# Performance work log

Hardware: AMD Instinct MI355X
Metric: run time of the kernel (lower is better)

The kernel has to match this reference:

```python
import jax, jax.numpy as jnp
import numpy as np

B, C, N, D = 8, 4, 1024, 96
H, DK, DV = 3, 32, 32
EPS = 1e-5


def setup_inputs() -> dict:
    key = jax.random.key(0)
    ks = jax.random.split(key, 7)
    s = 1.0 / np.sqrt(D)
    return {
        "input_Q": jax.random.normal(ks[0], (B, C, N, D), jnp.float32),
        "input_K": jax.random.normal(ks[1], (B, C, N, D), jnp.float32),
        "input_V": jax.random.normal(ks[2], (B, C, N, D), jnp.float32),
        "W_Q": jax.random.normal(ks[3], (H * DK, D), jnp.float32) * s,
        "W_K": jax.random.normal(ks[4], (H * DK, D), jnp.float32) * s,
        "W_V": jax.random.normal(ks[5], (H * DV, D), jnp.float32) * s,
        "W_fc": jax.random.normal(ks[6], (D, H * DV), jnp.float32) * s,
        "ln_gamma": jnp.ones((D,), jnp.float32),
        "ln_beta": jnp.zeros((D,), jnp.float32),
    }


def reference(input_Q, input_K, input_V, W_Q, W_K, W_V, W_fc, ln_gamma, ln_beta):
    # projections (torch Linear: x @ W.T), then split heads: [B,C,N,H*dk] -> [B,C,H,N,dk]
    def split_heads(x, W, dh):
        y = jnp.einsum('bcnd,ed->bcne', x, W)
        return y.reshape(B, C, N, H, dh).transpose(0, 1, 3, 2, 4)

    Q = split_heads(input_Q, W_Q, DK)
    K = split_heads(input_K, W_K, DK)
    V = split_heads(input_V, W_V, DV)

    scores = jnp.einsum('bchqd,bchkd->bchqk', Q, K) / np.sqrt(DK).astype(np.float32)
    # NOTE: original code softmaxes over dim=3 of the 5D scores == the QUERY axis
    attn = jax.nn.softmax(scores, axis=3)
    context = jnp.einsum('bchqk,bchkd->bchqd', attn, V)
    context = context.transpose(0, 1, 3, 2, 4).reshape(B, C, N, H * DV)

    out = jnp.einsum('bcne,de->bcnd', context, W_fc) + input_Q  # residual
    mu = jnp.mean(out, axis=-1, keepdims=True)
    var = jnp.var(out, axis=-1, keepdims=True)
    return (out - mu) * jax.lax.rsqrt(var + EPS) * ln_gamma + ln_beta
```

## Files before the change

kernel.cpp:

```cpp
#include <hip/hip_runtime.h>
#include <hip/hip_bf16.h>

#define NB 8
#define NC 4
#define NN 1024
#define ND 96
#define NHH 3
#define DKV 32
#define NBC (NB*NC)
#define NHEAD (NBC*NHH)
#define NROWS (NBC*NN)
#define C1 0.25503486910638953f
#define EPSV 1e-5f

using short8 = __attribute__((ext_vector_type(8))) short;
using sh4    = __attribute__((ext_vector_type(4))) short;
using f32x4  = __attribute__((ext_vector_type(4))) float;
using f32x16 = __attribute__((ext_vector_type(16))) float;

__device__ __forceinline__ short bf16_of(float f) {
  __hip_bfloat16 h = __float2bfloat16(f);
  return __builtin_bit_cast(short, h);
}
__device__ __forceinline__ float f_of_bf16(short s) {
  return __bfloat162float(__builtin_bit_cast(__hip_bfloat16, s));
}

__device__ __forceinline__ short8 load_cvt8(const float* p) {
  float4 f0 = *(const float4*)p;
  float4 f1 = *(const float4*)(p + 4);
  short8 v;
  v[0] = bf16_of(f0.x); v[1] = bf16_of(f0.y); v[2] = bf16_of(f0.z); v[3] = bf16_of(f0.w);
  v[4] = bf16_of(f1.x); v[5] = bf16_of(f1.y); v[6] = bf16_of(f1.z); v[7] = bf16_of(f1.w);
  return v;
}

__device__ __forceinline__ void gload_lds16(const void* g, void* l) {
  __builtin_amdgcn_global_load_lds(
      (const __attribute__((address_space(1))) unsigned int*)g,
      (__attribute__((address_space(3))) unsigned int*)l,
      16, 0, 0);
}

__global__ __launch_bounds__(256) void proj_kernel(
    const float* __restrict__ xq, const float* __restrict__ xk, const float* __restrict__ xv,
    const float* __restrict__ Wq, const float* __restrict__ Wk, const float* __restrict__ Wv,
    short* __restrict__ qb, short* __restrict__ kb, short* __restrict__ vb)
{
  __shared__ __align__(16) short wlds[96][104];
  __shared__ __align__(16) short xlds[64][104];
  const int t = threadIdx.x;
  const int p = blockIdx.x >> 9;
  const int blkrow0 = (blockIdx.x & 511) * 64;

  const float* x = (p == 0) ? xq : (p == 1) ? xk : xv;
  const float* W = (p == 0) ? Wq : (p == 1) ? Wk : Wv;
  short* dst = (p == 0) ? qb : (p == 1) ? kb : vb;
  const float sc = (p == 1) ? C1 : 1.0f;

#pragma unroll
  for (int i = 0; i < 9; ++i) {
    const int idx = i*256 + t;
    const float4 wv = *(const float4*)(W + (size_t)idx*4);
    const int f = idx*4, row = f/96, col = f%96;
    sh4 w4;
    w4[0] = bf16_of(wv.x); w4[1] = bf16_of(wv.y);
    w4[2] = bf16_of(wv.z); w4[3] = bf16_of(wv.w);
    *(sh4*)&wlds[row][col] = w4;
  }
#pragma unroll
  for (int it = 0; it < 3; ++it) {
    const int f = it*2048 + t*8;
    const int row = f / 96, col = f % 96;
    *(short8*)&xlds[row][col] = load_cvt8(x + (size_t)(blkrow0 + row)*ND + col);
  }
  __syncthreads();

  const int wave = t >> 6, lane = t & 63;
  const int g = lane >> 4, li = lane & 15;
  const int acol = g * 8;

  const short8 a0 = *(const short8*)&xlds[wave*16 + li][acol];
  const short8 a1 = *(const short8*)&xlds[wave*16 + li][32 + acol];
  const short8 a2 = *(const short8*)&xlds[wave*16 + li][64 + acol];

  f32x4 oacc[6];
#pragma unroll
  for (int tt = 0; tt < 6; ++tt) {
    f32x4 acc = {0.f, 0.f, 0.f, 0.f};
    const short* wr = &wlds[tt*16 + li][acol];
    acc = __builtin_amdgcn_mfma_f32_16x16x32_bf16(a0, *(const short8*)(wr),      acc, 0, 0, 0);
    acc = __builtin_amdgcn_mfma_f32_16x16x32_bf16(a1, *(const short8*)(wr + 32), acc, 0, 0, 0);
    acc = __builtin_amdgcn_mfma_f32_16x16x32_bf16(a2, *(const short8*)(wr + 64), acc, 0, 0, 0);
    oacc[tt] = acc;
  }

#pragma unroll
  for (int tt = 0; tt < 6; ++tt)
#pragma unroll
    for (int r = 0; r < 4; ++r)
      xlds[wave*16 + g*4 + r][tt*16 + li] = bf16_of(oacc[tt][r] * sc);
  __syncthreads();

#pragma unroll
  for (int it = 0; it < 3; ++it) {
    const int task = it*256 + t;
    const int nn_l = task / 12, seg = task - nn_l*12;
    const int col8 = seg*8;
    const int h = col8 >> 5, dd = col8 & 31;
    const int n = blkrow0 + nn_l;
    const int bcx = n >> 10, nnx = n & 1023;
    *(short8*)&dst[((size_t)(bcx*NHH + h)*NN + nnx)*DKV + dd] =
        *(const short8*)&xlds[nn_l][col8];
  }
}

__global__ __launch_bounds__(256) void stats_kernel(
    const short* __restrict__ qb, const short* __restrict__ kb,
    const short* __restrict__ vb, short* __restrict__ vtb)
{
  __shared__ __align__(16) short s_q[2][4096];
  __shared__ float s_is[128];
  __shared__ __align__(16) short s_t[32][128];

  const int t = threadIdx.x, wave = t >> 6, lane = t & 63;
  const int g = lane >> 4, li = lane & 15;
  const int head = blockIdx.x % NHEAD;
  const int kblk = blockIdx.x / NHEAD;
  const int kb0 = kblk*128;
  const int k0 = kb0 + wave*32;

  const short* kr = kb + ((size_t)head*NN + k0)*DKV + g*8;
  const short8 af0 = *(const short8*)(kr + (size_t)li*DKV);
  const short8 af1 = *(const short8*)(kr + (size_t)(16 + li)*DKV);

  const int nl = t >> 1;
  const int dvs = (t & 1) * 16;
  const short* vrow = vb + ((size_t)head*NN + kb0 + nl)*DKV + dvs;
  const short8 v0 = *(const short8*)(vrow);
  const short8 v1 = *(const short8*)(vrow + 8);

  const char* qsrc = (const char*)(qb + (size_t)head*NN*DKV);
  char* sq0 = (char*)&s_q[0][0];
  char* sq1 = (char*)&s_q[1][0];
  const int wseg = wave*2048;

  f32x4 s0 = {0.f,0.f,0.f,0.f}, s1 = {0.f,0.f,0.f,0.f};

#pragma unroll
  for (int j = 0; j < 2; ++j)
    gload_lds16(qsrc + wseg + j*1024 + lane*16, sq0 + wseg + j*1024);
  __syncthreads();

  for (int qc = 0; qc < 8; ++qc) {
    const int cur = qc & 1;
    const short* scur = (const short*)(cur ? sq1 : sq0);
    char* snxt = cur ? sq0 : sq1;
    if (qc < 7) {
#pragma unroll
      for (int j = 0; j < 2; ++j)
        gload_lds16(qsrc + (size_t)(qc+1)*8192 + wseg + j*1024 + lane*16,
                    snxt + wseg + j*1024);
    }
    __builtin_amdgcn_s_setprio(1);
#pragma unroll
    for (int qt = 0; qt < 8; ++qt) {
      const short8 bf = *(const short8*)(scur + (qt*16 + li)*32 + g*8);
      f32x4 z = {0.f,0.f,0.f,0.f};
      f32x4 d0 = __builtin_amdgcn_mfma_f32_16x16x32_bf16(af0, bf, z, 0, 0, 0);
      f32x4 d1 = __builtin_amdgcn_mfma_f32_16x16x32_bf16(af1, bf, z, 0, 0, 0);
#pragma unroll
      for (int r = 0; r < 4; ++r) {
        s0[r] += __builtin_amdgcn_exp2f(d0[r]);
        s1[r] += __builtin_amdgcn_exp2f(d1[r]);
      }
    }
    __builtin_amdgcn_s_setprio(0);
    __syncthreads();
  }

#pragma unroll
  for (int ms = 1; ms <= 8; ms <<= 1) {
#pragma unroll
    for (int r = 0; r < 4; ++r) {
      s0[r] += __shfl_xor(s0[r], ms);
      s1[r] += __shfl_xor(s1[r], ms);
    }
  }
  if (li == 0) {
    float* dst = s_is + wave*32 + g*4;
#pragma unroll
    for (int r = 0; r < 4; ++r) {
      dst[r]      = 1.0f / s0[r];
      dst[16 + r] = 1.0f / s1[r];
    }
  }
  __syncthreads();

  {
    const float isv = s_is[nl];
    short* st = &s_t[0][0];
#pragma unroll
    for (int j = 0; j < 8; ++j) {
      const int dv0 = dvs + j, dv1 = dvs + 8 + j;
      st[dv0*128 + (((nl*2) ^ ((dv0 & 7) << 4)) >> 1)] = bf16_of(isv * f_of_bf16(v0[j]));
      st[dv1*128 + (((nl*2) ^ ((dv1 & 7) << 4)) >> 1)] = bf16_of(isv * f_of_bf16(v1[j]));
    }
  }
  __syncthreads();

  {
    const short* st = &s_t[0][0];
#pragma unroll
    for (int it = 0; it < 2; ++it) {
      const int task = it*256 + t;
      const int dv = task >> 4, ns = task & 15;
      short8 v = *(const short8*)(st + dv*128 + (((ns*16) ^ ((dv & 7) << 4)) >> 1));
      *(short8*)(vtb + ((size_t)head*DKV + dv)*NN + kb0 + ns*8) = v;
    }
  }
}

__global__ __launch_bounds__(384) void ctxout_kernel(
    const short* __restrict__ qb, const short* __restrict__ kb,
    const short* __restrict__ vtb, const float* __restrict__ resid,
    const float* __restrict__ Wfc, const float* __restrict__ gamma,
    const float* __restrict__ beta, float* __restrict__ out)
{
  __shared__ __align__(16) char smem[49152];

  const int t = threadIdx.x;
  const int w = t >> 6, lane = t & 63;
  const int li = lane & 31, hi = lane >> 5;
  const int hs = t >> 7;
  const int sub = w & 1;
  const int bc = blockIdx.x % NBC;
  const int qtile = blockIdx.x / NBC;
  const int q0 = qtile*64 + sub*32;
  const int head = bc*NHH + hs;

  float4 wreg[6];
#pragma unroll
  for (int i = 0; i < 6; ++i)
    wreg[i] = *(const float4*)(Wfc + i*1536 + t*4);

  char* kbase = smem + hs*16384;
  char* vbase = kbase + 8192;

  const short* kgp = kb  + (size_t)head*NN*DKV;
  const short* vgp = vtb + (size_t)head*DKV*NN;
  const short* qrow = qb + ((size_t)head*NN + q0 + li)*DKV;
  const short8 qf0 = *(const short8*)(qrow + hi*8);
  const short8 qf1 = *(const short8*)(qrow + 16 + hi*8);

  int kgoff[2], vgoff[2], ldsseg[2];
#pragma unroll
  for (int j = 0; j < 2; ++j) {
    const int b = (sub*2 + j)*1024 + lane*16;
    const int r = b >> 7, c = b & 127;
    const int pc = c ^ ((r & 7) << 4);
    const int xk6 = r + 32*(pc >> 6);
    const int kr = (xk6 & 51) | ((xk6 & 4) << 1) | ((xk6 & 8) >> 1);
    kgoff[j] = kr*64 + (pc & 63);
    vgoff[j] = r*(NN*2) + pc;
    ldsseg[j] = (sub*2 + j)*1024;
  }

  int rd_off[2][2];
#pragma unroll
  for (int kt = 0; kt < 2; ++kt) {
    const int base = kt*64 + hi*16;
    rd_off[kt][0] = li*128 + ((base)      ^ ((li & 7) << 4));
    rd_off[kt][1] = li*128 + ((base + 32) ^ ((li & 7) << 4));
  }

  f32x16 acc = {0.f,0.f,0.f,0.f,0.f,0.f,0.f,0.f,0.f,0.f,0.f,0.f,0.f,0.f,0.f,0.f};

#pragma unroll
  for (int j = 0; j < 2; ++j) {
    gload_lds16((const char*)kgp + kgoff[j], kbase + ldsseg[j]);
    gload_lds16((const char*)vgp + vgoff[j], vbase + ldsseg[j]);
  }
  __syncthreads();

  for (int kc = 0; kc < 16; ++kc) {
    const int cur = kc & 1;
    if (kc < 15) {
      const size_t kadv = (size_t)(kc+1)*4096;
      const int vadv = (kc+1)*128;
#pragma unroll
      for (int j = 0; j < 2; ++j) {
        gload_lds16((const char*)kgp + kadv + kgoff[j],
                    kbase + (cur^1)*4096 + ldsseg[j]);
        gload_lds16((const char*)vgp + vadv + vgoff[j],
                    vbase + (cur^1)*4096 + ldsseg[j]);
      }
    }
    const char* kc_b = kbase + cur*4096;
    const char* vc_b = vbase + cur*4096;

    __builtin_amdgcn_s_setprio(1);
#pragma unroll
    for (int kt = 0; kt < 2; ++kt) {
      const short8 a0 = *(const short8*)(kc_b + rd_off[kt][0]);
      const short8 a1 = *(const short8*)(kc_b + rd_off[kt][1]);
      f32x16 sT = {0.f,0.f,0.f,0.f,0.f,0.f,0.f,0.f,0.f,0.f,0.f,0.f,0.f,0.f,0.f,0.f};
      sT = __builtin_amdgcn_mfma_f32_32x32x16_bf16(a0, qf0, sT, 0, 0, 0);
      sT = __builtin_amdgcn_mfma_f32_32x32x16_bf16(a1, qf1, sT, 0, 0, 0);
      short8 pa0, pa1;
#pragma unroll
      for (int j = 0; j < 8; ++j) {
        pa0[j] = bf16_of(__builtin_amdgcn_exp2f(sT[j]));
        pa1[j] = bf16_of(__builtin_amdgcn_exp2f(sT[8 + j]));
      }
      const short8 vfa = *(const short8*)(vc_b + rd_off[kt][0]);
      const short8 vfb = *(const short8*)(vc_b + rd_off[kt][1]);
      acc = __builtin_amdgcn_mfma_f32_32x32x16_bf16(pa0, vfa, acc, 0, 0, 0);
      acc = __builtin_amdgcn_mfma_f32_32x32x16_bf16(pa1, vfb, acc, 0, 0, 0);
    }
    __builtin_amdgcn_s_setprio(0);

    __syncthreads();
  }

  short* s_ct = (short*)smem;
  short* wlds = (short*)(smem + 13312);

#pragma unroll
  for (int reg = 0; reg < 16; ++reg) {
    const int ql = sub*32 + (reg & 3) + 8*(reg >> 2) + 4*hi;
    s_ct[ql*104 + hs*32 + li] = bf16_of(acc[reg]);
  }
#pragma unroll
  for (int i = 0; i < 6; ++i) {
    const int f = i*1536 + t*4;
    const int row = f / 96, col = f % 96;
    sh4 w4;
    w4[0] = bf16_of(wreg[i].x); w4[1] = bf16_of(wreg[i].y);
    w4[2] = bf16_of(wreg[i].z); w4[3] = bf16_of(wreg[i].w);
    *(sh4*)&wlds[row*104 + col] = w4;
  }
  __syncthreads();

  if (w < 4) {
    const int g16 = lane >> 4, li16 = lane & 15;
    const int rbase = w*16;
    const size_t rowg = (size_t)bc*NN + qtile*64 + rbase;

    const short* ar = s_ct + (rbase + li16)*104 + g16*8;
    const short8 a0 = *(const short8*)(ar);
    const short8 a1 = *(const short8*)(ar + 32);
    const short8 a2 = *(const short8*)(ar + 64);

    float o[6][4];
#pragma unroll
    for (int tt = 0; tt < 6; ++tt) {
      f32x4 oa = {0.f, 0.f, 0.f, 0.f};
      const short* wr = wlds + (tt*16 + li16)*104 + g16*8;
      oa = __builtin_amdgcn_mfma_f32_16x16x32_bf16(a0, *(const short8*)(wr),      oa, 0, 0, 0);
      oa = __builtin_amdgcn_mfma_f32_16x16x32_bf16(a1, *(const short8*)(wr + 32), oa, 0, 0, 0);
      oa = __builtin_amdgcn_mfma_f32_16x16x32_bf16(a2, *(const short8*)(wr + 64), oa, 0, 0, 0);
#pragma unroll
      for (int r = 0; r < 4; ++r)
        o[tt][r] = oa[r] + resid[(rowg + g16*4 + r)*ND + tt*16 + li16];
    }

    float s1v[4], s2v[4];
#pragma unroll
    for (int r = 0; r < 4; ++r) {
      float a = 0.f, b = 0.f;
#pragma unroll
      for (int tt = 0; tt < 6; ++tt) { a += o[tt][r]; b += o[tt][r]*o[tt][r]; }
      s1v[r] = a; s2v[r] = b;
    }
#pragma unroll
    for (int ms = 1; ms <= 8; ms <<= 1) {
#pragma unroll
      for (int r = 0; r < 4; ++r) {
        s1v[r] += __shfl_xor(s1v[r], ms);
        s2v[r] += __shfl_xor(s2v[r], ms);
      }
    }
    float mean[4], rs[4];
#pragma unroll
    for (int r = 0; r < 4; ++r) {
      mean[r] = s1v[r] * (1.0f/96.0f);
      float var = s2v[r]*(1.0f/96.0f) - mean[r]*mean[r];
      rs[r] = rsqrtf(var + EPSV);
    }
#pragma unroll
    for (int tt = 0; tt < 6; ++tt) {
      const int e = tt*16 + li16;
      const float gg = gamma[e], bb = beta[e];
#pragma unroll
      for (int r = 0; r < 4; ++r)
        out[(rowg + g16*4 + r)*ND + e] = (o[tt][r] - mean[r])*rs[r]*gg + bb;
    }
  }
}

extern "C" void kernel_launch(void* const* d_in, const int* in_sizes, int n_in,
                              void* d_out, int out_size, void* d_ws, size_t ws_size,
                              hipStream_t stream) {
  (void)in_sizes; (void)n_in; (void)out_size; (void)ws_size;
  const float* xq    = (const float*)d_in[0];
  const float* xk    = (const float*)d_in[1];
  const float* xv    = (const float*)d_in[2];
  const float* Wq    = (const float*)d_in[3];
  const float* Wk    = (const float*)d_in[4];
  const float* Wv    = (const float*)d_in[5];
  const float* Wfc   = (const float*)d_in[6];
  const float* gamma = (const float*)d_in[7];
  const float* beta  = (const float*)d_in[8];
  float* out = (float*)d_out;

  short* qb  = (short*)d_ws;
  short* kb  = qb  + (size_t)NHEAD*NN*DKV;
  short* vtb = kb  + (size_t)NHEAD*NN*DKV;
  short* vb  = vtb + (size_t)NHEAD*NN*DKV;

  hipLaunchKernelGGL(proj_kernel,   dim3(3*NROWS/64), dim3(256), 0, stream,
                     xq, xk, xv, Wq, Wk, Wv, qb, kb, vb);
  hipLaunchKernelGGL(stats_kernel,  dim3(NHEAD*8), dim3(256), 0, stream,
                     qb, kb, vb, vtb);
  hipLaunchKernelGGL(ctxout_kernel, dim3(NBC*16), dim3(384), 0, stream,
                     qb, kb, vtb, xq, Wfc, gamma, beta, out);
}
```

Measured before the change: 56.58 us.

## Triple-buffer K/V tiles in ctxout with prefetch distance two and vmcnt waits

Moves the attention-context kernel from double to triple buffering of K and V tiles in LDS, prefetching two chunks ahead. The full __syncthreads is replaced by a partial s_waitcnt vmcnt plus s_barrier, so one chunk's loads can stay in flight across the barrier. LDS per block grows from 48 KB to 72 KB through dynamic shared memory, which can lower the number of resident blocks per CU. Empty asm constraints pin the Wfc and Q registers so they are loaded early.

```diff
diff --git a/kernel.cpp b/kernel.cpp
--- a/kernel.cpp
+++ b/kernel.cpp
@@ -227,7 +227,7 @@
     const float* __restrict__ Wfc, const float* __restrict__ gamma,
     const float* __restrict__ beta, float* __restrict__ out)
 {
-  __shared__ __align__(16) char smem[49152];
+  extern __shared__ __align__(16) char smem[];
 
   const int t = threadIdx.x;
   const int w = t >> 6, lane = t & 63;
@@ -239,19 +239,23 @@
   const int q0 = qtile*64 + sub*32;
   const int head = bc*NHH + hs;
 
-  float4 wreg[6];
+  f32x4 wreg[6];
 #pragma unroll
   for (int i = 0; i < 6; ++i)
-    wreg[i] = *(const float4*)(Wfc + i*1536 + t*4);
-
-  char* kbase = smem + hs*16384;
-  char* vbase = kbase + 8192;
+    wreg[i] = *(const f32x4*)(Wfc + i*1536 + t*4);
+
+  char* kbase = smem + hs*24576;
+  char* vbase = kbase + 12288;
 
   const short* kgp = kb  + (size_t)head*NN*DKV;
   const short* vgp = vtb + (size_t)head*DKV*NN;
   const short* qrow = qb + ((size_t)head*NN + q0 + li)*DKV;
-  const short8 qf0 = *(const short8*)(qrow + hi*8);
-  const short8 qf1 = *(const short8*)(qrow + 16 + hi*8);
+  short8 qf0 = *(const short8*)(qrow + hi*8);
+  short8 qf1 = *(const short8*)(qrow + 16 + hi*8);
+
+#pragma unroll
+  for (int i = 0; i < 6; ++i) asm volatile("" : "+v"(wreg[i]));
+  asm volatile("" : "+v"(qf0), "+v"(qf1));
 
   int kgoff[2], vgoff[2], ldsseg[2];
 #pragma unroll
@@ -277,23 +281,30 @@
   f32x16 acc = {0.f,0.f,0.f,0.f,0.f,0.f,0.f,0.f,0.f,0.f,0.f,0.f,0.f,0.f,0.f,0.f};
 
 #pragma unroll
-  for (int j = 0; j < 2; ++j) {
-    gload_lds16((const char*)kgp + kgoff[j], kbase + ldsseg[j]);
-    gload_lds16((const char*)vgp + vgoff[j], vbase + ldsseg[j]);
-  }
-  __syncthreads();
+  for (int c = 0; c < 2; ++c) {
+    const size_t kadv = (size_t)c*4096;
+    const int vadv = c*128;
+#pragma unroll
+    for (int j = 0; j < 2; ++j) {
+      gload_lds16((const char*)kgp + kadv + kgoff[j], kbase + c*4096 + ldsseg[j]);
+      gload_lds16((const char*)vgp + vadv + vgoff[j], vbase + c*4096 + ldsseg[j]);
+    }
+  }
+  __builtin_amdgcn_sched_barrier(0);
+  asm volatile("s_waitcnt vmcnt(4)" ::: "memory");
+  __builtin_amdgcn_s_barrier();
+  __builtin_amdgcn_sched_barrier(0);
 
   for (int kc = 0; kc < 16; ++kc) {
-    const int cur = kc & 1;
-    if (kc < 15) {
-      const size_t kadv = (size_t)(kc+1)*4096;
-      const int vadv = (kc+1)*128;
+    const int cur = kc % 3;
+    if (kc < 14) {
+      const int nb = (kc + 2) % 3;
+      const size_t kadv = (size_t)(kc+2)*4096;
+      const int vadv = (kc+2)*128;
 #pragma unroll
       for (int j = 0; j < 2; ++j) {
-        gload_lds16((const char*)kgp + kadv + kgoff[j],
-                    kbase + (cur^1)*4096 + ldsseg[j]);
-        gload_lds16((const char*)vgp + vadv + vgoff[j],
-                    vbase + (cur^1)*4096 + ldsseg[j]);
+        gload_lds16((const char*)kgp + kadv + kgoff[j], kbase + nb*4096 + ldsseg[j]);
+        gload_lds16((const char*)vgp + vadv + vgoff[j], vbase + nb*4096 + ldsseg[j]);
       }
     }
     const char* kc_b = kbase + cur*4096;
@@ -320,7 +331,11 @@
     }
     __builtin_amdgcn_s_setprio(0);
 
-    __syncthreads();
+    __builtin_amdgcn_sched_barrier(0);
+    if (kc < 14) asm volatile("s_waitcnt vmcnt(4)" ::: "memory");
+    else         asm volatile("s_waitcnt vmcnt(0)" ::: "memory");
+    __builtin_amdgcn_s_barrier();
+    __builtin_amdgcn_sched_barrier(0);
   }
 
   short* s_ct = (short*)smem;
@@ -336,8 +351,8 @@
     const int f = i*1536 + t*4;
     const int row = f / 96, col = f % 96;
     sh4 w4;
-    w4[0] = bf16_of(wreg[i].x); w4[1] = bf16_of(wreg[i].y);
-    w4[2] = bf16_of(wreg[i].z); w4[3] = bf16_of(wreg[i].w);
+    w4[0] = bf16_of(wreg[i][0]); w4[1] = bf16_of(wreg[i][1]);
+    w4[2] = bf16_of(wreg[i][2]); w4[3] = bf16_of(wreg[i][3]);
     *(sh4*)&wlds[row*104 + col] = w4;
   }
   __syncthreads();
@@ -419,10 +434,13 @@
   short* vtb = kb  + (size_t)NHEAD*NN*DKV;
   short* vb  = vtb + (size_t)NHEAD*NN*DKV;
 
+  hipFuncSetAttribute((const void*)ctxout_kernel,
+                      hipFuncAttributeMaxDynamicSharedMemorySize, 73728);
+
   hipLaunchKernelGGL(proj_kernel,   dim3(3*NROWS/64), dim3(256), 0, stream,
                      xq, xk, xv, Wq, Wk, Wv, qb, kb, vb);
   hipLaunchKernelGGL(stats_kernel,  dim3(NHEAD*8), dim3(256), 0, stream,
                      qb, kb, vb, vtb);
-  hipLaunchKernelGGL(ctxout_kernel, dim3(NBC*16), dim3(384), 0, stream,
+  hipLaunchKernelGGL(ctxout_kernel, dim3(NBC*16), dim3(384), 73728, stream,
                      qb, kb, vtb, xq, Wfc, gamma, beta, out);
 }
```

Result: no change. 57.38 us (+1.4%).
